# Optimization experiments

Hardware: AMD Instinct MI355X
Metric: run time of the kernel (lower is better)

## Reference

```python
import jax, jax.numpy as jnp
import numpy as np

MAX_SAMPLES = 400  # init max_samples
EPS = 1e-9


def setup_inputs() -> dict:
    key = jax.random.key(0)
    k1, k2, k3, k4 = jax.random.split(key, 4)
    E, N, K, L = 8192, 2048, 8, 16
    # per-edge probabilities (positive, as the loss takes log of ratios)
    probas = jax.random.uniform(k1, (E,), jnp.float32, minval=1e-3, maxval=1.0)
    # soft cluster assignments: row-normalized so Bhattacharyya coeff <= 1
    c = jax.random.uniform(k2, (N, K), jnp.float32)
    clusters = c / c.sum(axis=1, keepdims=True)
    edges_nn = jax.random.randint(k3, (E, 2), 0, N)
    label_keypoints = jax.random.randint(k4, (L,), 0, N)
    return {"probas": probas, "clusters": clusters,
            "edges_nn": edges_nn, "label_keypoints": label_keypoints}


def reference(probas, clusters, edges_nn, label_keypoints):
    E = edges_nn.shape[0]
    clst = jnp.argmax(clusters, axis=1)                      # [N] hard assignment
    c0 = clst[edges_nn[:, 0]]                                # [E]
    c1 = clst[edges_nn[:, 1]]                                # [E]
    assigned = clst[label_keypoints]                         # [L] clusters at keypoints
    # edge selected if either endpoint lies in a keypoint cluster (union over labels,
    # static-shape mask form of get_edges_on_location)
    sel = jnp.any((c0[None, :] == assigned[:, None]) |
                  (c1[None, :] == assigned[:, None]), axis=0)  # [E]
    sims = c0 == c1
    pos = sel & sims                                          # positive edges
    neg = sel & ~sims                                         # negative edges
    # Bhattacharyya coefficient per edge: sum_k sqrt(p_k * q_k)
    bc = jnp.sqrt(clusters[edges_nn[:, 0]] * clusters[edges_nn[:, 1]]).sum(axis=1)  # [E]
    # pos x neg cross product, restricted to pairs sharing the anchor node edges[.,0]
    same_anchor = edges_nn[:, 0][:, None] == edges_nn[None, :, 0]   # [E,E]
    valid = pos[:, None] & neg[None, :] & same_anchor               # [E,E]
    w = 1.0 - 0.5 * (bc[:, None] + bc[None, :])                     # [E,E] sampling prob
    logw = jnp.where(valid & (w > 0),
                     jnp.log(jnp.maximum(w, EPS)), -jnp.inf)
    # multinomial-without-replacement via Gumbel top-k (deterministic key)
    u = jax.random.uniform(jax.random.key(42), (E, E), jnp.float32)
    gumbel = -jnp.log(-jnp.log(u + EPS) + EPS)
    vals, flat_idx = jax.lax.top_k((logw + gumbel).reshape(-1), MAX_SAMPLES)
    i_ = flat_idx // E                                        # positive-edge rows
    j_ = flat_idx % E                                         # negative-edge rows
    p_pos = probas[i_]
    p_neg = probas[j_]
    term = jnp.log(p_pos / (p_pos + p_neg))                   # [max_samples]
    # guard against < max_samples valid pairs (torch would just sample fewer)
    ok = jnp.isfinite(vals)
    loss = -jnp.sum(jnp.where(ok, term, 0.0)) / jnp.maximum(jnp.sum(ok), 1)
    return loss
```

## Files before the change

### kernel.cpp

```cpp
#include <hip/hip_runtime.h>
#include <stdint.h>


#define E_CONST 8192
#define N_CONST 2048
#define K_CONST 8
#define L_CONST 16
#define MAXS 400
#define EPS_F 1e-9f
#define NTHR 1024
#define RCAP 4096

#define OFF_CLUA   0
#define OFF_CLUB   32768
#define OFF_PK     65536
#define OFF_Q      73728
#define OFF_CUR    81920
#define OFF_CSR    90112
#define OFF_EDGE   106496
#define OFF_CLST   139264
#define OFF_TMP    141312
#define OFF_HIST   141376
#define OFF_WSUM   142400
#define OFF_WCNT   142464
#define OFF_MISC   142528
#define LDS_BYTES  142592

struct Cand { float val; uint32_t pack; };

__device__ __forceinline__ uint2 threefry2x32_42(uint32_t x0, uint32_t x1) {
    const uint32_t ks0 = 0u, ks1 = 42u;
    const uint32_t ks2 = ks0 ^ ks1 ^ 0x1BD11BDAu;
    const uint32_t ks[3] = {ks0, ks1, ks2};
    const int R[2][4] = {{13, 15, 26, 6}, {17, 29, 16, 24}};
    x0 += ks0; x1 += ks1;
#pragma unroll
    for (int g = 0; g < 5; ++g) {
        const int* r = R[g & 1];
#pragma unroll
        for (int q = 0; q < 4; ++q) {
            x0 += x1;
            x1 = (x1 << r[q]) | (x1 >> (32 - r[q]));
            x1 ^= x0;
        }
        x0 += ks[(g + 1) % 3];
        x1 += ks[(g + 2) % 3] + (uint32_t)(g + 1);
    }
    return make_uint2(x0, x1);
}

__device__ __forceinline__ float gumbel_at(uint32_t idx) {
    uint2 o = threefry2x32_42(0u, idx);
    uint32_t bits = o.x ^ o.y;
    float u = __uint_as_float((bits >> 9) | 0x3F800000u) - 1.0f;
    return -__logf(-__logf(u + EPS_F) + EPS_F);
}

__device__ __forceinline__ uint32_t sortable_key(float f) {
    uint32_t b = __float_as_uint(f);
    return (b & 0x80000000u) ? ~b : (b | 0x80000000u);
}

__device__ __forceinline__ int argmax8(float4 a, float4 b) {
    float v[8] = {a.x, a.y, a.z, a.w, b.x, b.y, b.z, b.w};
    float best = v[0]; int bi = 0;
#pragma unroll
    for (int k = 1; k < 8; ++k)
        if (v[k] > best) { best = v[k]; bi = k; }
    return bi;
}

__device__ __forceinline__ void scan_inplace(int* arr, int* tmp, int* totalOut) {
    int tid = threadIdx.x;
    int lane = tid & 63, wid = tid >> 6;
    int i0 = 2 * tid, i1 = i0 + 1;
    int v0 = arr[i0], v1 = arr[i1];
    int s = v0 + v1;
    int inc = s;
#pragma unroll
    for (int off = 1; off < 64; off <<= 1) {
        int u = __shfl_up(inc, off);
        if (lane >= off) inc += u;
    }
    if (lane == 63) tmp[wid] = inc;
    __syncthreads();
    if (wid == 0) {
        int w = (lane < 16) ? tmp[lane] : 0;
        int incw = w;
#pragma unroll
        for (int off = 1; off < 16; off <<= 1) {
            int u = __shfl_up(incw, off);
            if (lane >= off) incw += u;
        }
        if (lane < 16) tmp[lane] = incw - w;
    }
    __syncthreads();
    int base = tmp[wid] + (inc - s);
    arr[i0] = base;
    arr[i1] = base + v0;
    if (tid == 1023) *totalOut = base + v0 + v1;
    __syncthreads();
}

__global__ __launch_bounds__(1024) void k_all(
    const float* __restrict__ probas, const float* __restrict__ clusters,
    const int* __restrict__ edges, const int* __restrict__ keypts,
    Cand* __restrict__ spill, int pmax, float* __restrict__ out) {

    extern __shared__ char smem[];
    float4*   s_cluA = (float4*)(smem + OFF_CLUA);
    float4*   s_cluB = (float4*)(smem + OFF_CLUB);
    int*      s_pk   = (int*)(smem + OFF_PK);
    int*      s_q    = (int*)(smem + OFF_Q);
    int*      s_cur  = (int*)(smem + OFF_CUR);
    uint16_t* s_csr  = (uint16_t*)(smem + OFF_CSR);
    uint32_t* s_edge = (uint32_t*)(smem + OFF_EDGE);
    uint8_t*  s_clst = (uint8_t*)(smem + OFF_CLST);
    int*      s_tmp  = (int*)(smem + OFF_TMP);
    int*      s_hist = (int*)(smem + OFF_HIST);
    float*    s_wsum = (float*)(smem + OFF_WSUM);
    int*      s_wcnt = (int*)(smem + OFF_WCNT);
    int*      s_misc = (int*)(smem + OFF_MISC);

    int tid = threadIdx.x;
    int lane = tid & 63;

    const int2* ed2 = (const int2*)edges;
    int2 pre[8];
#pragma unroll
    for (int it = 0; it < 8; ++it) pre[it] = ed2[tid + it * NTHR];

    s_pk[tid] = 0; s_pk[tid + 1024] = 0;
    if (tid == 0) s_misc[0] = 0;

    const float4* c4 = (const float4*)clusters;
#pragma unroll
    for (int r = 0; r < 2; ++r) {
        int n = tid + r * 1024;
        float4 a = c4[2 * n], b = c4[2 * n + 1];
        s_cluA[n] = a; s_cluB[n] = b;
        s_clst[n] = (uint8_t)argmax8(a, b);
    }
    __syncthreads();
    if (tid < L_CONST)
        atomicOr((uint32_t*)&s_misc[0], 1u << s_clst[keypts[tid]]);
    __syncthreads();
    uint32_t m = (uint32_t)s_misc[0];

    uint32_t af[8];
#pragma unroll
    for (int it = 0; it < 8; ++it) {
        int e = tid + it * NTHR;
        int2 p = pre[it];
        s_edge[e] = ((uint32_t)p.x << 16) | (uint32_t)p.y;
        int c0 = s_clst[p.x], c1 = s_clst[p.y];
        int f = 0;
        if ((((m >> c0) | (m >> c1)) & 1u)) f = (c0 == c1) ? 1 : 2;
        af[it] = ((uint32_t)p.x << 2) | (uint32_t)f;
        if (f == 1)      atomicAdd(&s_pk[p.x], 1);
        else if (f == 2) atomicAdd(&s_pk[p.x], 0x10000);
    }
    __syncthreads();

    {
        int i0 = 2 * tid, i1 = i0 + 1;
        int p0 = s_pk[i0], p1 = s_pk[i1];
        s_q[i0] = (p0 & 0xFFFF) * (p0 >> 16);
        s_q[i1] = (p1 & 0xFFFF) * (p1 >> 16);
    }
    __syncthreads();
    scan_inplace(s_pk, s_tmp, &s_misc[1]);
    scan_inplace(s_q, s_tmp, &s_misc[2]);
    s_cur[2 * tid] = s_pk[2 * tid];
    s_cur[2 * tid + 1] = s_pk[2 * tid + 1];
    __syncthreads();
    int nPosTot = s_misc[1] & 0xFFFF;
    int nNegTot = s_misc[1] >> 16;
    int P = s_misc[2]; if (P > pmax) P = pmax;

#pragma unroll
    for (int it = 0; it < 8; ++it) {
        int f = (int)(af[it] & 3u);
        int a = (int)(af[it] >> 2);
        int e = tid + it * NTHR;
        if (f == 1) {
            int old = atomicAdd(&s_cur[a], 1);
            s_csr[old & 0xFFFF] = (uint16_t)e;
        } else if (f == 2) {
            int old = atomicAdd(&s_cur[a], 0x10000);
            s_csr[nPosTot + (old >> 16)] = (uint16_t)e;
        }
    }
    __syncthreads();

    auto bc_of = [&](int e) -> float {
        uint32_t pe = s_edge[e];
        int n0 = (int)(pe >> 16), n1 = (int)(pe & 0xFFFFu);
        float4 a0 = s_cluA[n0], a1 = s_cluB[n0];
        float4 b0 = s_cluA[n1], b1 = s_cluB[n1];
        float s = __builtin_amdgcn_sqrtf(a0.x * b0.x);
        s += __builtin_amdgcn_sqrtf(a0.y * b0.y);
        s += __builtin_amdgcn_sqrtf(a0.z * b0.z);
        s += __builtin_amdgcn_sqrtf(a0.w * b0.w);
        s += __builtin_amdgcn_sqrtf(a1.x * b1.x);
        s += __builtin_amdgcn_sqrtf(a1.y * b1.y);
        s += __builtin_amdgcn_sqrtf(a1.z * b1.z);
        s += __builtin_amdgcn_sqrtf(a1.w * b1.w);
        return s;
    };
    auto make_cand = [&](int t, float& val, uint32_t& pack) {
        int lo = 0, hi = N_CONST - 1;
#pragma unroll
        for (int itr = 0; itr < 11; ++itr) {
            int mid = (lo + hi + 1) >> 1;
            if (s_q[mid] <= t) lo = mid; else hi = mid - 1;
        }
        int a = lo;
        int loc = t - s_q[a];
        int pk = s_pk[a];
        int pb = pk & 0xFFFF, nb = pk >> 16;
        int nextN = (a < N_CONST - 1) ? (s_pk[a + 1] >> 16) : nNegTot;
        int nn = nextN - nb;
        int ip = loc / nn;
        int jn = loc - ip * nn;
        int i = s_csr[pb + ip];
        int j = s_csr[nPosTot + nb + jn];
        float w = 1.0f - 0.5f * (bc_of(i) + bc_of(j));
        val = (w > 0.0f)
            ? __logf(fmaxf(w, EPS_F)) + gumbel_at((uint32_t)i * E_CONST + (uint32_t)j)
            : -INFINITY;
        pack = ((uint32_t)i << 16) | (uint32_t)j;
    };

    float vval0 = 0.f, vval1 = 0.f, vval2 = 0.f, vval3 = 0.f;
    uint32_t vpk0 = 0, vpk1 = 0, vpk2 = 0, vpk3 = 0;
    if (tid        < P) make_cand(tid,        vval0, vpk0);
    if (tid + 1024 < P) make_cand(tid + 1024, vval1, vpk1);
    if (tid + 2048 < P) make_cand(tid + 2048, vval2, vpk2);
    if (tid + 3072 < P) make_cand(tid + 3072, vval3, vpk3);
    for (int t = tid + RCAP; t < P; t += NTHR) {
        float v; uint32_t pk;
        make_cand(t, v, pk);
        spill[t - RCAP].val = v; spill[t - RCAP].pack = pk;
    }
    uint32_t vk0 = sortable_key(vval0), vk1 = sortable_key(vval1);
    uint32_t vk2 = sortable_key(vval2), vk3 = sortable_key(vval3);
    __syncthreads();

    uint32_t* s_prefix = (uint32_t*)&s_misc[3];
    int*      s_target = &s_misc[4];
    int M = P;
    uint32_t thr = 0;
    if (M > MAXS) {
        if (tid == 0) { *s_prefix = 0; *s_target = MAXS; }
        __syncthreads();
        for (int pass = 0; pass < 4; ++pass) {
            int shift = 24 - 8 * pass;
            if (tid < 256) s_hist[tid] = 0;
            __syncthreads();
            uint32_t pfx = *s_prefix;
            auto hist_add = [&](bool inRange, uint32_t k) {
                bool act = inRange && (pass == 0 || (k >> (shift + 8)) == pfx);
                uint32_t b = (k >> shift) & 255u;
                uint32_t v = act ? b : 256u;
                uint64_t peers = ~0ull;
#pragma unroll
                for (int bit = 0; bit < 9; ++bit) {
                    uint64_t vote = __ballot((v >> bit) & 1u);
                    peers &= ((v >> bit) & 1u) ? vote : ~vote;
                }
                if (act) {
                    int leader = __ffsll((unsigned long long)peers) - 1;
                    if (lane == leader) atomicAdd(&s_hist[b], (int)__popcll(peers));
                }
            };
            hist_add(tid        < M, vk0);
            hist_add(tid + 1024 < M, vk1);
            hist_add(tid + 2048 < M, vk2);
            hist_add(tid + 3072 < M, vk3);
            for (int t = tid + RCAP; t < M; t += NTHR) {
                uint32_t k = sortable_key(spill[t - RCAP].val);
                if (pass == 0 || (k >> (shift + 8)) == pfx)
                    atomicAdd(&s_hist[(k >> shift) & 255], 1);
            }
            __syncthreads();
            if (tid < 64) {
                int h0 = s_hist[4 * tid], h1 = s_hist[4 * tid + 1];
                int h2 = s_hist[4 * tid + 2], h3 = s_hist[4 * tid + 3];
                int sincl = h0 + h1 + h2 + h3;
#pragma unroll
                for (int off = 1; off < 64; off <<= 1) {
                    int v = __shfl_down(sincl, off);
                    if (tid + off < 64) sincl += v;
                }
                int excl = __shfl_down(sincl, 1);
                if (tid == 63) excl = 0;
                int suf3 = excl + h3;
                int suf2 = suf3 + h2;
                int suf1 = suf2 + h1;
                int suf0 = suf1 + h0;
                int tgt = *s_target;
                uint32_t pfxOld = *s_prefix;
                if      (suf0 >= tgt && suf1 < tgt) { *s_prefix = (pfxOld << 8) | (4u*tid+0); *s_target = tgt - suf1; }
                else if (suf1 >= tgt && suf2 < tgt) { *s_prefix = (pfxOld << 8) | (4u*tid+1); *s_target = tgt - suf2; }
                else if (suf2 >= tgt && suf3 < tgt) { *s_prefix = (pfxOld << 8) | (4u*tid+2); *s_target = tgt - suf3; }
                else if (suf3 >= tgt && excl < tgt) { *s_prefix = (pfxOld << 8) | (4u*tid+3); *s_target = tgt - excl; }
            }
            __syncthreads();
        }
        thr = *s_prefix;
    }

    float mysum = 0.f;
    int myc = 0;
    auto accum = [&](int t, float v, uint32_t k, uint32_t pk) {
        if (t < M && v != -INFINITY && k >= thr) {
            int i = (int)(pk >> 16), j = (int)(pk & 0xFFFFu);
            float pi = probas[i], pj = probas[j];
            mysum += __logf(pi / (pi + pj));
            myc++;
        }
    };
    accum(tid,        vval0, vk0, vpk0);
    accum(tid + 1024, vval1, vk1, vpk1);
    accum(tid + 2048, vval2, vk2, vpk2);
    accum(tid + 3072, vval3, vk3, vpk3);
    for (int t = tid + RCAP; t < M; t += NTHR) {
        Cand c = spill[t - RCAP];
        accum(t, c.val, sortable_key(c.val), c.pack);
    }
#pragma unroll
    for (int off = 32; off > 0; off >>= 1) {
        mysum += __shfl_down(mysum, off);
        myc   += __shfl_down(myc, off);
    }
    int wid = tid >> 6;
    if ((tid & 63) == 0) { s_wsum[wid] = mysum; s_wcnt[wid] = myc; }
    __syncthreads();
    if (tid == 0) {
        float s = 0.f; int c = 0;
        for (int w = 0; w < 16; ++w) { s += s_wsum[w]; c += s_wcnt[w]; }
        if (c < 1) c = 1;
        out[0] = -s / (float)c;
    }
}

extern "C" void kernel_launch(void* const* d_in, const int* in_sizes, int n_in,
                              void* d_out, int out_size, void* d_ws, size_t ws_size,
                              hipStream_t stream) {
    const float* probas   = (const float*)d_in[0];
    const float* clusters = (const float*)d_in[1];
    const int*   edges    = (const int*)d_in[2];
    const int*   keypts   = (const int*)d_in[3];
    float* out = (float*)d_out;

    Cand* spill = (Cand*)d_ws;
    int spill_cap = (int)(ws_size / sizeof(Cand));
    if (spill_cap > 61440) spill_cap = 61440;
    int pmax = RCAP + spill_cap;

    hipFuncSetAttribute((const void*)k_all,
                        hipFuncAttributeMaxDynamicSharedMemorySize, LDS_BYTES);

    k_all<<<1, NTHR, LDS_BYTES, stream>>>(probas, clusters, edges, keypts,
                                          spill, pmax, out);
}
```

Before: 28.00 us.

## Precompute per-edge Bhattacharyya coefficients, tabulate pair owner, simplify histogram atomics

Computes each edge's Bhattacharyya coefficient once during edge classification and stores it in LDS. Candidate generation then reads two floats instead of recomputing sixteen sqrt products. Adds an LDS table mapping each pair index to its anchor node, replacing the 11-step binary search for indices below a cap. The ballot-based warp-aggregated histogram is replaced with plain LDS atomics. This trades extra up-front bc work on all 8192 edges and more LDS for cheaper per-candidate work; plain atomics may contend more on hot bins.

After: 26.22 us. 6.3% less time.

```diff
diff --git a/kernel.cpp b/kernel.cpp
--- a/kernel.cpp
+++ b/kernel.cpp
@@ -10,6 +10,7 @@
 #define EPS_F 1e-9f
 #define NTHR 1024
 #define RCAP 4096
+#define TCAP 6144
 
 #define OFF_CLUA   0
 #define OFF_CLUB   32768
@@ -17,14 +18,15 @@
 #define OFF_Q      73728
 #define OFF_CUR    81920
 #define OFF_CSR    90112
-#define OFF_EDGE   106496
+#define OFF_BC     106496
 #define OFF_CLST   139264
-#define OFF_TMP    141312
-#define OFF_HIST   141376
-#define OFF_WSUM   142400
-#define OFF_WCNT   142464
-#define OFF_MISC   142528
-#define LDS_BYTES  142592
+#define OFF_PA     141312
+#define OFF_TMP    153600
+#define OFF_HIST   153664
+#define OFF_WSUM   154688
+#define OFF_WCNT   154752
+#define OFF_MISC   154816
+#define LDS_BYTES  154848
 
 struct Cand { float val; uint32_t pack; };
 
@@ -114,8 +116,9 @@
     int*      s_q    = (int*)(smem + OFF_Q);
     int*      s_cur  = (int*)(smem + OFF_CUR);
     uint16_t* s_csr  = (uint16_t*)(smem + OFF_CSR);
-    uint32_t* s_edge = (uint32_t*)(smem + OFF_EDGE);
+    float*    s_bc   = (float*)(smem + OFF_BC);
     uint8_t*  s_clst = (uint8_t*)(smem + OFF_CLST);
+    uint16_t* s_pa   = (uint16_t*)(smem + OFF_PA);
     int*      s_tmp  = (int*)(smem + OFF_TMP);
     int*      s_hist = (int*)(smem + OFF_HIST);
     float*    s_wsum = (float*)(smem + OFF_WSUM);
@@ -123,7 +126,6 @@
     int*      s_misc = (int*)(smem + OFF_MISC);
 
     int tid = threadIdx.x;
-    int lane = tid & 63;
 
     const int2* ed2 = (const int2*)edges;
     int2 pre[8];
@@ -152,13 +154,23 @@
     for (int it = 0; it < 8; ++it) {
         int e = tid + it * NTHR;
         int2 p = pre[it];
-        s_edge[e] = ((uint32_t)p.x << 16) | (uint32_t)p.y;
         int c0 = s_clst[p.x], c1 = s_clst[p.y];
         int f = 0;
         if ((((m >> c0) | (m >> c1)) & 1u)) f = (c0 == c1) ? 1 : 2;
         af[it] = ((uint32_t)p.x << 2) | (uint32_t)f;
         if (f == 1)      atomicAdd(&s_pk[p.x], 1);
         else if (f == 2) atomicAdd(&s_pk[p.x], 0x10000);
+        float4 a0 = s_cluA[p.x], a1 = s_cluB[p.x];
+        float4 b0 = s_cluA[p.y], b1 = s_cluB[p.y];
+        float s = __builtin_amdgcn_sqrtf(a0.x * b0.x);
+        s += __builtin_amdgcn_sqrtf(a0.y * b0.y);
+        s += __builtin_amdgcn_sqrtf(a0.z * b0.z);
+        s += __builtin_amdgcn_sqrtf(a0.w * b0.w);
+        s += __builtin_amdgcn_sqrtf(a1.x * b1.x);
+        s += __builtin_amdgcn_sqrtf(a1.y * b1.y);
+        s += __builtin_amdgcn_sqrtf(a1.z * b1.z);
+        s += __builtin_amdgcn_sqrtf(a1.w * b1.w);
+        s_bc[e] = s;
     }
     __syncthreads();
 
@@ -176,7 +188,8 @@
     __syncthreads();
     int nPosTot = s_misc[1] & 0xFFFF;
     int nNegTot = s_misc[1] >> 16;
-    int P = s_misc[2]; if (P > pmax) P = pmax;
+    int totQ = s_misc[2];
+    int P = totQ; if (P > pmax) P = pmax;
 
 #pragma unroll
     for (int it = 0; it < 8; ++it) {
@@ -191,31 +204,25 @@
             s_csr[nPosTot + (old >> 16)] = (uint16_t)e;
         }
     }
-    __syncthreads();
-
-    auto bc_of = [&](int e) -> float {
-        uint32_t pe = s_edge[e];
-        int n0 = (int)(pe >> 16), n1 = (int)(pe & 0xFFFFu);
-        float4 a0 = s_cluA[n0], a1 = s_cluB[n0];
-        float4 b0 = s_cluA[n1], b1 = s_cluB[n1];
-        float s = __builtin_amdgcn_sqrtf(a0.x * b0.x);
-        s += __builtin_amdgcn_sqrtf(a0.y * b0.y);
-        s += __builtin_amdgcn_sqrtf(a0.z * b0.z);
-        s += __builtin_amdgcn_sqrtf(a0.w * b0.w);
-        s += __builtin_amdgcn_sqrtf(a1.x * b1.x);
-        s += __builtin_amdgcn_sqrtf(a1.y * b1.y);
-        s += __builtin_amdgcn_sqrtf(a1.z * b1.z);
-        s += __builtin_amdgcn_sqrtf(a1.w * b1.w);
-        return s;
-    };
+    for (int a = tid; a < N_CONST; a += NTHR) {
+        int q0 = s_q[a];
+        int q1 = (a < N_CONST - 1) ? s_q[a + 1] : totQ;
+        for (int t = q0; t < q1 && t < TCAP; ++t) s_pa[t] = (uint16_t)a;
+    }
+    __syncthreads();
+
     auto make_cand = [&](int t, float& val, uint32_t& pack) {
-        int lo = 0, hi = N_CONST - 1;
-#pragma unroll
-        for (int itr = 0; itr < 11; ++itr) {
-            int mid = (lo + hi + 1) >> 1;
-            if (s_q[mid] <= t) lo = mid; else hi = mid - 1;
-        }
-        int a = lo;
+        int a;
+        if (t < TCAP) a = (int)s_pa[t];
+        else {
+            int lo = 0, hi = N_CONST - 1;
+#pragma unroll
+            for (int itr = 0; itr < 11; ++itr) {
+                int mid = (lo + hi + 1) >> 1;
+                if (s_q[mid] <= t) lo = mid; else hi = mid - 1;
+            }
+            a = lo;
+        }
         int loc = t - s_q[a];
         int pk = s_pk[a];
         int pb = pk & 0xFFFF, nb = pk >> 16;
@@ -225,7 +232,7 @@
         int jn = loc - ip * nn;
         int i = s_csr[pb + ip];
         int j = s_csr[nPosTot + nb + jn];
-        float w = 1.0f - 0.5f * (bc_of(i) + bc_of(j));
+        float w = 1.0f - 0.5f * (s_bc[i] + s_bc[j]);
         val = (w > 0.0f)
             ? __logf(fmaxf(w, EPS_F)) + gumbel_at((uint32_t)i * E_CONST + (uint32_t)j)
             : -INFINITY;
@@ -259,25 +266,10 @@
             if (tid < 256) s_hist[tid] = 0;
             __syncthreads();
             uint32_t pfx = *s_prefix;
-            auto hist_add = [&](bool inRange, uint32_t k) {
-                bool act = inRange && (pass == 0 || (k >> (shift + 8)) == pfx);
-                uint32_t b = (k >> shift) & 255u;
-                uint32_t v = act ? b : 256u;
-                uint64_t peers = ~0ull;
-#pragma unroll
-                for (int bit = 0; bit < 9; ++bit) {
-                    uint64_t vote = __ballot((v >> bit) & 1u);
-                    peers &= ((v >> bit) & 1u) ? vote : ~vote;
-                }
-                if (act) {
-                    int leader = __ffsll((unsigned long long)peers) - 1;
-                    if (lane == leader) atomicAdd(&s_hist[b], (int)__popcll(peers));
-                }
-            };
-            hist_add(tid        < M, vk0);
-            hist_add(tid + 1024 < M, vk1);
-            hist_add(tid + 2048 < M, vk2);
-            hist_add(tid + 3072 < M, vk3);
+            if (tid        < M && (pass == 0 || (vk0 >> (shift + 8)) == pfx)) atomicAdd(&s_hist[(vk0 >> shift) & 255], 1);
+            if (tid + 1024 < M && (pass == 0 || (vk1 >> (shift + 8)) == pfx)) atomicAdd(&s_hist[(vk1 >> shift) & 255], 1);
+            if (tid + 2048 < M && (pass == 0 || (vk2 >> (shift + 8)) == pfx)) atomicAdd(&s_hist[(vk2 >> shift) & 255], 1);
+            if (tid + 3072 < M && (pass == 0 || (vk3 >> (shift + 8)) == pfx)) atomicAdd(&s_hist[(vk3 >> shift) & 255], 1);
             for (int t = tid + RCAP; t < M; t += NTHR) {
                 uint32_t k = sortable_key(spill[t - RCAP].val);
                 if (pass == 0 || (k >> (shift + 8)) == pfx)
```
